# Performance work log

Hardware: AMD Instinct MI355X
Metric: run time of the kernel (lower is better)

Reference implementation:

```python
import math
import jax
import jax.numpy as jnp
import numpy as np

KS = 7  # kernel_size


def _make_cdt_kernel():
    # kornia.create_meshgrid(k,k,normalized=False) -> coords; centered; hypot -> exp(d/-0.35)
    r = np.arange(KS, dtype=np.float32) - (KS // 2)
    yy, xx = np.meshgrid(r, r, indexing="ij")
    k = np.exp(np.hypot(xx, yy) / -0.35)
    return jnp.asarray(k, jnp.float32)[None, None]  # (1,1,KS,KS) OIHW


def setup_inputs() -> dict:
    key = jax.random.key(0)
    B, C, H, W = 32, 3, 256, 256
    u = jax.random.uniform(key, (B, C, H, W), dtype=jnp.float32)
    image = (u < 0.005).astype(jnp.float32)
    return {"image": image}


def reference(image):
    B, C, H, W = image.shape
    kernel = _make_cdt_kernel()
    n_iters = math.ceil(max(H, W) / (KS // 2))  # static
    x = image.reshape(B * C, 1, H, W)
    out0 = jnp.zeros_like(x)

    def step(carry, i):
        out, boundary = carry
        conv = jax.lax.conv_general_dilated(
            boundary, kernel, (1, 1), "SAME",
            dimension_numbers=("NCHW", "OIHW", "NCHW"))
        # -0.35*log(conv) with posinf (conv==0) replaced by 0, exactly as
        # torch.nan_to_num(cdt, posinf=0.0); safe-log form avoids inf/nan.
        pos = conv > 0
        cdt = jnp.where(pos, -0.35 * jnp.log(jnp.where(pos, conv, 1.0)), 0.0)
        mask = cdt > 0
        offset = i.astype(jnp.float32) * (KS / 2)  # i * kernel_size / 2 (true div)
        out = out + jnp.where(mask, offset + cdt, 0.0)
        boundary = jnp.where(mask, 1.0, boundary)
        return (out, boundary), None

    (out, _), _ = jax.lax.scan(step, (out0, x), jnp.arange(n_iters))
    return out.reshape(B, C, H, W)
```

## Files before the change

kernel.cpp:

```cpp
#include <hip/hip_runtime.h>


typedef unsigned short u16x4 __attribute__((ext_vector_type(4)));

#define BIGV (1 << 20)
#define ROWB 272
#define CHB (256 * ROWB)

__global__ __launch_bounds__(256) void k_rowdist(const float* __restrict__ img,
                                                 unsigned char* __restrict__ d1) {
  const int lane = threadIdx.x & 63;
  const int wv = threadIdx.x >> 6;
  const int row = blockIdx.x * 4 + wv;
  const int x0 = lane * 4;

  const float4 v = *reinterpret_cast<const float4*>(&img[(size_t)row * 256 + x0]);

  int c0 = (v.x != 0.0f) ? -x0 : BIGV;
  int c1 = (v.y != 0.0f) ? -(x0 + 1) : BIGV;
  int c2 = (v.z != 0.0f) ? -(x0 + 2) : BIGV;
  int c3 = (v.w != 0.0f) ? -(x0 + 3) : BIGV;
  const int p0 = c0;
  const int p1 = min(c1, p0);
  const int p2 = min(c2, p1);
  const int p3 = min(c3, p2);
  int incl = p3;
#pragma unroll
  for (int off = 1; off < 64; off <<= 1) {
    int o = __shfl_up(incl, off, 64);
    if (lane >= off) incl = min(incl, o);
  }
  int excl = __shfl_up(incl, 1, 64);
  if (lane == 0) excl = BIGV;
  const int df0 = x0 + min(p0, excl);
  const int df1 = x0 + 1 + min(p1, excl);
  const int df2 = x0 + 2 + min(p2, excl);
  const int df3 = x0 + 3 + min(p3, excl);

  int g0 = (v.x != 0.0f) ? x0 : BIGV;
  int g1 = (v.y != 0.0f) ? (x0 + 1) : BIGV;
  int g2 = (v.z != 0.0f) ? (x0 + 2) : BIGV;
  int g3 = (v.w != 0.0f) ? (x0 + 3) : BIGV;
  const int q3 = g3;
  const int q2 = min(g2, q3);
  const int q1 = min(g1, q2);
  const int q0 = min(g0, q1);
  int incl2 = q0;
#pragma unroll
  for (int off = 1; off < 64; off <<= 1) {
    int o = __shfl_down(incl2, off, 64);
    if (lane < 64 - off) incl2 = min(incl2, o);
  }
  int excl2 = __shfl_down(incl2, 1, 64);
  if (lane == 63) excl2 = BIGV;
  const int db0 = min(q0, excl2) - x0;
  const int db1 = min(q1, excl2) - (x0 + 1);
  const int db2 = min(q2, excl2) - (x0 + 2);
  const int db3 = min(q3, excl2) - (x0 + 3);

  const unsigned int d0 = (unsigned int)min(min(df0, db0), 127);
  const unsigned int d1v = (unsigned int)min(min(df1, db1), 127);
  const unsigned int d2 = (unsigned int)min(min(df2, db2), 127);
  const unsigned int d3 = (unsigned int)min(min(df3, db3), 127);
  const int ch = row >> 8, y = row & 255;
  const size_t base = (size_t)ch * CHB + (size_t)y * ROWB;
  *reinterpret_cast<unsigned int*>(&d1[base + 8 + x0]) =
      d0 | (d1v << 8) | (d2 << 16) | (d3 << 24);
  if (lane < 2)
    *reinterpret_cast<unsigned int*>(&d1[base + lane * 4]) = 0u;
  else if (lane >= 62)
    *reinterpret_cast<unsigned int*>(&d1[base + 264 + (lane - 62) * 4]) = 0u;
}

#define TAPROW(s_, t_, A0, A1, A2, A3, A4, A5, A6)                              \
  do {                                                                          \
    const unsigned int r0_ = R[(s_) + (t_)][0];                                 \
    const unsigned int r1_ = R[(s_) + (t_)][1];                                 \
    const unsigned int r2_ = R[(s_) + (t_)][2];                                 \
    A0 += (((__builtin_amdgcn_alignbyte(r1_, r0_, 1) + Cp) & 0x80808080u) >> 7);\
    A1 += (((__builtin_amdgcn_alignbyte(r1_, r0_, 2) + Cp) & 0x80808080u) >> 7);\
    A2 += (((__builtin_amdgcn_alignbyte(r1_, r0_, 3) + Cp) & 0x80808080u) >> 7);\
    A3 += (((r1_ + Cp) & 0x80808080u) >> 7);                                    \
    A4 += (((__builtin_amdgcn_alignbyte(r2_, r1_, 1) + Cp) & 0x80808080u) >> 7);\
    A5 += (((__builtin_amdgcn_alignbyte(r2_, r1_, 2) + Cp) & 0x80808080u) >> 7);\
    A6 += (((__builtin_amdgcn_alignbyte(r2_, r1_, 3) + Cp) & 0x80808080u) >> 7);\
  } while (0)

#define TAPROWC(s_, t_, A0, A1, A2, A4, A5, A6)   \
  do {                                                                          \
    const unsigned int r0_ = R[(s_) + (t_)][0];                                 \
    const unsigned int r1_ = R[(s_) + (t_)][1];                                 \
    const unsigned int r2_ = R[(s_) + (t_)][2];                                 \
    A0 += (((__builtin_amdgcn_alignbyte(r1_, r0_, 1) + Cp) & 0x80808080u) >> 7);\
    A1 += (((__builtin_amdgcn_alignbyte(r1_, r0_, 2) + Cp) & 0x80808080u) >> 7);\
    A2 += (((__builtin_amdgcn_alignbyte(r1_, r0_, 3) + Cp) & 0x80808080u) >> 7);\
    A4 += (((__builtin_amdgcn_alignbyte(r2_, r1_, 1) + Cp) & 0x80808080u) >> 7);\
    A5 += (((__builtin_amdgcn_alignbyte(r2_, r1_, 2) + Cp) & 0x80808080u) >> 7);\
    A6 += (((__builtin_amdgcn_alignbyte(r2_, r1_, 3) + Cp) & 0x80808080u) >> 7);\
  } while (0)

#define EPI(s_)                                                                 \
  do {                                                                          \
    const unsigned int Dc = R[(s_) + 3][1];                                     \
    const int d0_ = (int)(Dc & 255u);                                           \
    const int d1_ = (int)((Dc >> 8) & 255u);                                    \
    const int d2_ = (int)((Dc >> 16) & 255u);                                   \
    const int d3_ = (int)(Dc >> 24);                                            \
    const int i0_ = (max(d0_ - 1, 0) * 86) >> 8;      \
    const int i1_ = (max(d1_ - 1, 0) * 86) >> 8;                                \
    const int i2_ = (max(d2_ - 1, 0) * 86) >> 8;                                \
    const int i3_ = (max(d3_ - 1, 0) * 86) >> 8;                                \
    const unsigned int Cp = (unsigned int)(127 - 3 * i0_) |                     \
                            ((unsigned int)(127 - 3 * i1_) << 8) |              \
                            ((unsigned int)(127 - 3 * i2_) << 16) |             \
                            ((unsigned int)(127 - 3 * i3_) << 24);              \
    unsigned int aA = 0, aB = 0, aC = 0, aD = 0;                                \
    TAPROW(s_, 0, aD, aD, aC, aC, aC, aD, aD);                                  \
    TAPROW(s_, 1, aD, aC, aB, aB, aB, aC, aD);                                  \
    TAPROW(s_, 2, aC, aB, aA, aA, aA, aB, aC);                                  \
    TAPROWC(s_, 3, aC, aB, aA, aA, aB, aC);                                     \
    TAPROW(s_, 4, aC, aB, aA, aA, aA, aB, aC);                                  \
    TAPROW(s_, 5, aD, aC, aB, aB, aB, aC, aD);                                  \
    TAPROW(s_, 6, aD, aD, aC, aC, aC, aD, aD);                                  \
    const float s0_ = fmaf((float)(aA & 255u), wA,                              \
                     fmaf((float)(aB & 255u), wB,                               \
                     fmaf((float)(aC & 255u), wC, (float)(aD & 255u) * wD)));   \
    const float s1_ = fmaf((float)((aA >> 8) & 255u), wA,                       \
                     fmaf((float)((aB >> 8) & 255u), wB,                        \
                     fmaf((float)((aC >> 8) & 255u), wC,                        \
                          (float)((aD >> 8) & 255u) * wD)));                    \
    const float s2_ = fmaf((float)((aA >> 16) & 255u), wA,                      \
                     fmaf((float)((aB >> 16) & 255u), wB,                       \
                     fmaf((float)((aC >> 16) & 255u), wC,                       \
                          (float)((aD >> 16) & 255u) * wD)));                   \
    const float s3_ = fmaf((float)(aA >> 24), wA,                               \
                     fmaf((float)(aB >> 24), wB,                                \
                     fmaf((float)(aC >> 24), wC, (float)(aD >> 24) * wD)));     \
    const float cv0_ = W4 - s0_, cv1_ = W4 - s1_;                               \
    const float cv2_ = W4 - s2_, cv3_ = W4 - s3_;                               \
    const float e0_ = fmaf(3.5f, (float)i0_, -0.35f * __logf(fmaxf(cv0_, 1e-30f))); \
    const float e1_ = fmaf(3.5f, (float)i1_, -0.35f * __logf(fmaxf(cv1_, 1e-30f))); \
    const float e2_ = fmaf(3.5f, (float)i2_, -0.35f * __logf(fmaxf(cv2_, 1e-30f))); \
    const float e3_ = fmaf(3.5f, (float)i3_, -0.35f * __logf(fmaxf(cv3_, 1e-30f))); \
    const float4 o4_ = make_float4(                                             \
        (d0_ > 0 && cv0_ > 1e-6f) ? e0_ : 0.0f,                                 \
        (d1_ > 0 && cv1_ > 1e-6f) ? e1_ : 0.0f,                                 \
        (d2_ > 0 && cv2_ > 1e-6f) ? e2_ : 0.0f,                                 \
        (d3_ > 0 && cv3_ > 1e-6f) ? e3_ : 0.0f);                                \
    *reinterpret_cast<float4*>(&out[obase + (size_t)(s_) * 256]) = o4_;         \
  } while (0)

#define LDQ(off) (*reinterpret_cast<const u16x4*>(&s1[(off)]))
#define EMIN __builtin_elementwise_min
#define EMAX __builtin_elementwise_max

__global__ __launch_bounds__(256) void k_fused(const unsigned char* __restrict__ d1,
                                               float* __restrict__ out) {
  const int ch = blockIdx.z;
  const int yt = blockIdx.y;
  const int xt = blockIdx.x;
  const int x0 = xt * 32;
  const int y0 = yt * 128;
  const int tid = threadIdx.x;
  const int lastxt = (int)gridDim.x - 1;

  __shared__ __align__(16) unsigned char s1[256 * 96];
  __shared__ __align__(16) unsigned char Ds[134 * 44];

  const unsigned char* src = d1 + (size_t)ch * CHB + x0;
#pragma unroll
  for (int it = 0; it < 3; ++it) {
    const int idx = it * 256 + tid;
    const int y = (idx * 21846) >> 16;
    const int seg = idx - y * 3;
    const uint4 q = *reinterpret_cast<const uint4*>(&src[y * ROWB + seg * 16]);
    uint4 lo, hi;
    lo.x = __builtin_amdgcn_perm(0u, q.x, 0x0C010C00u);
    lo.y = __builtin_amdgcn_perm(0u, q.x, 0x0C030C02u);
    lo.z = __builtin_amdgcn_perm(0u, q.y, 0x0C010C00u);
    lo.w = __builtin_amdgcn_perm(0u, q.y, 0x0C030C02u);
    hi.x = __builtin_amdgcn_perm(0u, q.z, 0x0C010C00u);
    hi.y = __builtin_amdgcn_perm(0u, q.z, 0x0C030C02u);
    hi.z = __builtin_amdgcn_perm(0u, q.w, 0x0C010C00u);
    hi.w = __builtin_amdgcn_perm(0u, q.w, 0x0C030C02u);
    *reinterpret_cast<uint4*>(&s1[y * 96 + seg * 32]) = lo;
    *reinterpret_cast<uint4*>(&s1[y * 96 + seg * 32 + 16]) = hi;
  }
  __syncthreads();

  const u16x4 K1 = {1, 1, 1, 1}, K2 = {2, 2, 2, 2}, K3 = {3, 3, 3, 3},
              K4 = {4, 4, 4, 4}, K5 = {5, 5, 5, 5}, K6 = {6, 6, 6, 6},
              K7 = {7, 7, 7, 7}, K8 = {8, 8, 8, 8};
#pragma unroll 1
  for (int it = 0; it < 6; ++it) {
    const int idx = it * 256 + tid;
    if (idx >= 1340) break;
    const int r = (idx * 6554) >> 16;
    const int g = idx - r * 10;
    const int y = y0 + r - 3;
    const bool ghost =
        (xt == 0 && g == 0) || (xt == lastxt && g == 9) || y < 0 || y > 255;
    if (ghost) {
      *reinterpret_cast<unsigned int*>(&Ds[r * 44 + g * 4]) = 0x7F7F7F7Fu;
      continue;
    }
    const int jb = 8 + 8 * g;
    const int rb = y * 96 + jb;
    const int bot = 255 * 96 + jb;
    const u16x4 b0 = LDQ(rb);
    const u16x4 u1 = LDQ(max(rb - 96, jb));
    const u16x4 u2 = LDQ(max(rb - 192, jb));
    const u16x4 u3 = LDQ(max(rb - 288, jb));
    const u16x4 u4 = LDQ(max(rb - 384, jb));
    const u16x4 u5 = LDQ(max(rb - 480, jb));
    const u16x4 u6 = LDQ(max(rb - 576, jb));
    const u16x4 u7 = LDQ(max(rb - 672, jb));
    const u16x4 u8 = LDQ(max(rb - 768, jb));
    const u16x4 w1 = LDQ(min(rb + 96, bot));
    const u16x4 w2 = LDQ(min(rb + 192, bot));
    const u16x4 w3 = LDQ(min(rb + 288, bot));
    const u16x4 w4 = LDQ(min(rb + 384, bot));
    const u16x4 w5 = LDQ(min(rb + 480, bot));
    const u16x4 w6 = LDQ(min(rb + 576, bot));
    const u16x4 w7 = LDQ(min(rb + 672, bot));
    const u16x4 w8 = LDQ(min(rb + 768, bot));
    const u16x4 mu = EMIN(EMIN(EMIN(EMAX(u1, K1), EMAX(u2, K2)),
                                EMIN(EMAX(u3, K3), EMAX(u4, K4))),
                          EMIN(EMIN(EMAX(u5, K5), EMAX(u6, K6)),
                                EMIN(EMAX(u7, K7), EMAX(u8, K8))));
    const u16x4 mw = EMIN(EMIN(EMIN(EMAX(w1, K1), EMAX(w2, K2)),
                                EMIN(EMAX(w3, K3), EMAX(w4, K4))),
                          EMIN(EMIN(EMAX(w5, K5), EMAX(w6, K6)),
                                EMIN(EMAX(w7, K7), EMAX(w8, K8))));
    u16x4 b = EMIN(b0, EMIN(mu, mw));
    unsigned long long bb = __builtin_bit_cast(unsigned long long, b);
    unsigned int blo = (unsigned int)bb, bhi = (unsigned int)(bb >> 32);
    int bm = max(max((int)(blo & 0xFFFFu), (int)(blo >> 16)),
                 max((int)(bhi & 0xFFFFu), (int)(bhi >> 16)));
    int k = 9;
    int au = rb - 768, ad = rb + 768;
    while (k < bm) {
      const unsigned short t1 = (unsigned short)k, t2 = (unsigned short)(k + 1),
                           t3 = (unsigned short)(k + 2), t4 = (unsigned short)(k + 3);
      const u16x4 c1 = {t1, t1, t1, t1}, c2 = {t2, t2, t2, t2},
                  c3 = {t3, t3, t3, t3}, c4 = {t4, t4, t4, t4};
      const u16x4 a1 = LDQ(max(au - 96, jb));
      const u16x4 a2 = LDQ(max(au - 192, jb));
      const u16x4 a3 = LDQ(max(au - 288, jb));
      const u16x4 a4 = LDQ(max(au - 384, jb));
      const u16x4 e1 = LDQ(min(ad + 96, bot));
      const u16x4 e2 = LDQ(min(ad + 192, bot));
      const u16x4 e3 = LDQ(min(ad + 288, bot));
      const u16x4 e4 = LDQ(min(ad + 384, bot));
      const u16x4 t = EMIN(EMIN(EMIN(EMAX(a1, c1), EMAX(a2, c2)),
                                 EMIN(EMAX(a3, c3), EMAX(a4, c4))),
                           EMIN(EMIN(EMAX(e1, c1), EMAX(e2, c2)),
                                 EMIN(EMAX(e3, c3), EMAX(e4, c4))));
      b = EMIN(b, t);
      au -= 384;
      ad += 384;
      k += 4;
      bb = __builtin_bit_cast(unsigned long long, b);
      blo = (unsigned int)bb;
      bhi = (unsigned int)(bb >> 32);
      bm = max(max((int)(blo & 0xFFFFu), (int)(blo >> 16)),
               max((int)(bhi & 0xFFFFu), (int)(bhi >> 16)));
    }
    const unsigned int packed = __builtin_amdgcn_perm(bhi, blo, 0x06040200u);
    *reinterpret_cast<unsigned int*>(&Ds[r * 44 + g * 4]) = packed;
  }
  __syncthreads();

  const float wA = 3.17814e-2f, wB = 2.35426e-3f, wC = 1.91126e-4f, wD = 1.35150e-5f;
  const float W4 = 8.0f * wA + 12.0f * wB + 16.0f * wC + 12.0f * wD;

  const int cg = tid & 7;
  const int rg = tid >> 3;
  const int rl0 = rg * 4;
  const int jb2 = cg * 4;
  const size_t obase = (size_t)ch * 65536 + (size_t)(y0 + rl0) * 256 + x0 + cg * 4;

  unsigned int R[10][3];
#pragma unroll
  for (int u = 0; u < 10; ++u) {
    const unsigned char* p = &Ds[(rl0 + u) * 44 + jb2];
    R[u][0] = *reinterpret_cast<const unsigned int*>(p);
    R[u][1] = *reinterpret_cast<const unsigned int*>(p + 4);
    R[u][2] = *reinterpret_cast<const unsigned int*>(p + 8);
  }

  EPI(0); EPI(1); EPI(2); EPI(3);
}

extern "C" void kernel_launch(void* const* d_in, const int* in_sizes, int n_in,
                              void* d_out, int out_size, void* d_ws, size_t ws_size,
                              hipStream_t stream) {
  const float* img = (const float*)d_in[0];
  float* out = (float*)d_out;
  unsigned char* Dbuf = (unsigned char*)d_ws;

  const int total = in_sizes[0];
  const int nch = total >> 16;

  k_rowdist<<<dim3(nch * 64), dim3(256), 0, stream>>>(img, Dbuf);
  k_fused<<<dim3(8, 2, nch), dim3(256), 0, stream>>>(Dbuf, out);
}
```

Baseline: 45.93 us.

## Compute five column-distance rows per thread with shared sliding window loads

The vertical min-distance pass now has each thread handle five consecutive output rows. It loads a 21-row window of LDS data once and reuses it across the five rows, where before it did 17 separate loads per row. The LDS buffer gets padded ghost rows filled with a sentinel so the clamped max/min addressing is mostly gone. The trade is more registers and a larger LDS footprint, and the loop now runs 270 work items instead of 1340, which may leave many threads idle.

```diff
diff --git a/kernel.cpp b/kernel.cpp
--- a/kernel.cpp
+++ b/kernel.cpp
@@ -86,7 +86,7 @@
     A6 += (((__builtin_amdgcn_alignbyte(r2_, r1_, 3) + Cp) & 0x80808080u) >> 7);\
   } while (0)
 
-#define TAPROWC(s_, t_, A0, A1, A2, A4, A5, A6)   \
+#define TAPROWC(s_, t_, A0, A1, A2, A4, A5, A6)                                 \
   do {                                                                          \
     const unsigned int r0_ = R[(s_) + (t_)][0];                                 \
     const unsigned int r1_ = R[(s_) + (t_)][1];                                 \
@@ -106,7 +106,7 @@
     const int d1_ = (int)((Dc >> 8) & 255u);                                    \
     const int d2_ = (int)((Dc >> 16) & 255u);                                   \
     const int d3_ = (int)(Dc >> 24);                                            \
-    const int i0_ = (max(d0_ - 1, 0) * 86) >> 8;      \
+    const int i0_ = (max(d0_ - 1, 0) * 86) >> 8;                                \
     const int i1_ = (max(d1_ - 1, 0) * 86) >> 8;                                \
     const int i2_ = (max(d2_ - 1, 0) * 86) >> 8;                                \
     const int i3_ = (max(d3_ - 1, 0) * 86) >> 8;                                \
@@ -125,10 +125,10 @@
     const float s0_ = fmaf((float)(aA & 255u), wA,                              \
                      fmaf((float)(aB & 255u), wB,                               \
                      fmaf((float)(aC & 255u), wC, (float)(aD & 255u) * wD)));   \
-    const float s1_ = fmaf((float)((aA >> 8) & 255u), wA,                       \
-                     fmaf((float)((aB >> 8) & 255u), wB,                        \
-                     fmaf((float)((aC >> 8) & 255u), wC,                        \
-                          (float)((aD >> 8) & 255u) * wD)));                    \
+    const float s1f_ = fmaf((float)((aA >> 8) & 255u), wA,                      \
+                      fmaf((float)((aB >> 8) & 255u), wB,                       \
+                      fmaf((float)((aC >> 8) & 255u), wC,                       \
+                           (float)((aD >> 8) & 255u) * wD)));                   \
     const float s2_ = fmaf((float)((aA >> 16) & 255u), wA,                      \
                      fmaf((float)((aB >> 16) & 255u), wB,                       \
                      fmaf((float)((aC >> 16) & 255u), wC,                       \
@@ -136,7 +136,7 @@
     const float s3_ = fmaf((float)(aA >> 24), wA,                               \
                      fmaf((float)(aB >> 24), wB,                                \
                      fmaf((float)(aC >> 24), wC, (float)(aD >> 24) * wD)));     \
-    const float cv0_ = W4 - s0_, cv1_ = W4 - s1_;                               \
+    const float cv0_ = W4 - s0_, cv1_ = W4 - s1f_;                              \
     const float cv2_ = W4 - s2_, cv3_ = W4 - s3_;                               \
     const float e0_ = fmaf(3.5f, (float)i0_, -0.35f * __logf(fmaxf(cv0_, 1e-30f))); \
     const float e1_ = fmaf(3.5f, (float)i1_, -0.35f * __logf(fmaxf(cv1_, 1e-30f))); \
@@ -154,6 +154,33 @@
 #define EMIN __builtin_elementwise_min
 #define EMAX __builtin_elementwise_max
 
+#define PFX(OUT, a0, a1, a2, a3, a4, a5, a6, a7, a8, a9, a10, a11, a12, a13,    \
+            a14, a15, a16)                                                      \
+  u16x4 OUT = EMIN(                                                             \
+      EMIN(EMIN(EMIN(EMAX(a7, K1), EMAX(a9, K1)),                               \
+                EMIN(EMAX(a6, K2), EMAX(a10, K2))),                             \
+           EMIN(EMIN(EMAX(a5, K3), EMAX(a11, K3)),                              \
+                EMIN(EMAX(a4, K4), EMAX(a12, K4)))),                            \
+      EMIN(EMIN(EMIN(EMAX(a3, K5), EMAX(a13, K5)),                              \
+                EMIN(EMAX(a2, K6), EMAX(a14, K6))),                             \
+           EMIN(EMIN(EMAX(a1, K7), EMAX(a15, K7)),                              \
+                EMIN(EMAX(a0, K8), EMAX(a16, K8)))));                           \
+  OUT = EMIN(OUT, a8)
+
+#define TUP(OUT, b3, b2, b1, b0, d0, d1, d2, d3)                                \
+  OUT = EMIN(OUT, EMIN(EMIN(EMIN(EMAX(b3, Kc0), EMAX(b2, Kc1)),                 \
+                            EMIN(EMAX(b1, Kc2), EMAX(b0, Kc3))),                \
+                       EMIN(EMIN(EMAX(d0, Kc0), EMAX(d1, Kc1)),                 \
+                            EMIN(EMAX(d2, Kc2), EMAX(d3, Kc3)))))
+
+#define BMOF(MX)                                                                \
+  ({                                                                            \
+    const unsigned long long mb_ = __builtin_bit_cast(unsigned long long, MX);  \
+    const unsigned int ml_ = (unsigned int)mb_, mh_ = (unsigned int)(mb_ >> 32);\
+    max(max((int)(ml_ & 0xFFFFu), (int)(ml_ >> 16)),                            \
+        max((int)(mh_ & 0xFFFFu), (int)(mh_ >> 16)));                           \
+  })
+
 __global__ __launch_bounds__(256) void k_fused(const unsigned char* __restrict__ d1,
                                                float* __restrict__ out) {
   const int ch = blockIdx.z;
@@ -164,9 +191,15 @@
   const int tid = threadIdx.x;
   const int lastxt = (int)gridDim.x - 1;
 
-  __shared__ __align__(16) unsigned char s1[256 * 96];
-  __shared__ __align__(16) unsigned char Ds[134 * 44];
-
+  __shared__ __align__(16) unsigned char s1[279 * 96];
+  __shared__ __align__(16) unsigned char Ds[136 * 44];
+
+  for (int i = tid; i < 552; i += 256) {
+    const int r = (i * 2731) >> 16;
+    const int c = i - r * 24;
+    const int row = (r < 11) ? r : r + 256;
+    *reinterpret_cast<unsigned int*>(&s1[row * 96 + c * 4]) = 0x007F007Fu;
+  }
   const unsigned char* src = d1 + (size_t)ch * CHB + x0;
 #pragma unroll
   for (int it = 0; it < 3; ++it) {
@@ -183,8 +216,8 @@
     hi.y = __builtin_amdgcn_perm(0u, q.z, 0x0C030C02u);
     hi.z = __builtin_amdgcn_perm(0u, q.w, 0x0C010C00u);
     hi.w = __builtin_amdgcn_perm(0u, q.w, 0x0C030C02u);
-    *reinterpret_cast<uint4*>(&s1[y * 96 + seg * 32]) = lo;
-    *reinterpret_cast<uint4*>(&s1[y * 96 + seg * 32 + 16]) = hi;
+    *reinterpret_cast<uint4*>(&s1[(y + 11) * 96 + seg * 32]) = lo;
+    *reinterpret_cast<uint4*>(&s1[(y + 11) * 96 + seg * 32 + 16]) = hi;
   }
   __syncthreads();
 
@@ -192,82 +225,72 @@
               K4 = {4, 4, 4, 4}, K5 = {5, 5, 5, 5}, K6 = {6, 6, 6, 6},
               K7 = {7, 7, 7, 7}, K8 = {8, 8, 8, 8};
 #pragma unroll 1
-  for (int it = 0; it < 6; ++it) {
-    const int idx = it * 256 + tid;
-    if (idx >= 1340) break;
-    const int r = (idx * 6554) >> 16;
-    const int g = idx - r * 10;
-    const int y = y0 + r - 3;
-    const bool ghost =
-        (xt == 0 && g == 0) || (xt == lastxt && g == 9) || y < 0 || y > 255;
-    if (ghost) {
-      *reinterpret_cast<unsigned int*>(&Ds[r * 44 + g * 4]) = 0x7F7F7F7Fu;
+  for (int t = tid; t < 270; t += 256) {
+    const int rg5 = (t * 6554) >> 16;
+    const int g = t - rg5 * 10;
+    const int r0r = rg5 * 5;
+    const int ybase = y0 + r0r - 3;
+    const int dsb = r0r * 44 + g * 4;
+    if ((xt == 0 && g == 0) || (xt == lastxt && g == 9)) {
+      *reinterpret_cast<unsigned int*>(&Ds[dsb]) = 0x7F7F7F7Fu;
+      *reinterpret_cast<unsigned int*>(&Ds[dsb + 44]) = 0x7F7F7F7Fu;
+      *reinterpret_cast<unsigned int*>(&Ds[dsb + 88]) = 0x7F7F7F7Fu;
+      *reinterpret_cast<unsigned int*>(&Ds[dsb + 132]) = 0x7F7F7F7Fu;
+      *reinterpret_cast<unsigned int*>(&Ds[dsb + 176]) = 0x7F7F7F7Fu;
       continue;
     }
     const int jb = 8 + 8 * g;
-    const int rb = y * 96 + jb;
-    const int bot = 255 * 96 + jb;
-    const u16x4 b0 = LDQ(rb);
-    const u16x4 u1 = LDQ(max(rb - 96, jb));
-    const u16x4 u2 = LDQ(max(rb - 192, jb));
-    const u16x4 u3 = LDQ(max(rb - 288, jb));
-    const u16x4 u4 = LDQ(max(rb - 384, jb));
-    const u16x4 u5 = LDQ(max(rb - 480, jb));
-    const u16x4 u6 = LDQ(max(rb - 576, jb));
-    const u16x4 u7 = LDQ(max(rb - 672, jb));
-    const u16x4 u8 = LDQ(max(rb - 768, jb));
-    const u16x4 w1 = LDQ(min(rb + 96, bot));
-    const u16x4 w2 = LDQ(min(rb + 192, bot));
-    const u16x4 w3 = LDQ(min(rb + 288, bot));
-    const u16x4 w4 = LDQ(min(rb + 384, bot));
-    const u16x4 w5 = LDQ(min(rb + 480, bot));
-    const u16x4 w6 = LDQ(min(rb + 576, bot));
-    const u16x4 w7 = LDQ(min(rb + 672, bot));
-    const u16x4 w8 = LDQ(min(rb + 768, bot));
-    const u16x4 mu = EMIN(EMIN(EMIN(EMAX(u1, K1), EMAX(u2, K2)),
-                                EMIN(EMAX(u3, K3), EMAX(u4, K4))),
-                          EMIN(EMIN(EMAX(u5, K5), EMAX(u6, K6)),
-                                EMIN(EMAX(u7, K7), EMAX(u8, K8))));
-    const u16x4 mw = EMIN(EMIN(EMIN(EMAX(w1, K1), EMAX(w2, K2)),
-                                EMIN(EMAX(w3, K3), EMAX(w4, K4))),
-                          EMIN(EMIN(EMAX(w5, K5), EMAX(w6, K6)),
-                                EMIN(EMAX(w7, K7), EMAX(w8, K8))));
-    u16x4 b = EMIN(b0, EMIN(mu, mw));
-    unsigned long long bb = __builtin_bit_cast(unsigned long long, b);
-    unsigned int blo = (unsigned int)bb, bhi = (unsigned int)(bb >> 32);
-    int bm = max(max((int)(blo & 0xFFFFu), (int)(blo >> 16)),
-                 max((int)(bhi & 0xFFFFu), (int)(bhi >> 16)));
-    int k = 9;
-    int au = rb - 768, ad = rb + 768;
-    while (k < bm) {
-      const unsigned short t1 = (unsigned short)k, t2 = (unsigned short)(k + 1),
-                           t3 = (unsigned short)(k + 2), t4 = (unsigned short)(k + 3);
-      const u16x4 c1 = {t1, t1, t1, t1}, c2 = {t2, t2, t2, t2},
-                  c3 = {t3, t3, t3, t3}, c4 = {t4, t4, t4, t4};
-      const u16x4 a1 = LDQ(max(au - 96, jb));
-      const u16x4 a2 = LDQ(max(au - 192, jb));
-      const u16x4 a3 = LDQ(max(au - 288, jb));
-      const u16x4 a4 = LDQ(max(au - 384, jb));
-      const u16x4 e1 = LDQ(min(ad + 96, bot));
-      const u16x4 e2 = LDQ(min(ad + 192, bot));
-      const u16x4 e3 = LDQ(min(ad + 288, bot));
-      const u16x4 e4 = LDQ(min(ad + 384, bot));
-      const u16x4 t = EMIN(EMIN(EMIN(EMAX(a1, c1), EMAX(a2, c2)),
-                                 EMIN(EMAX(a3, c3), EMAX(a4, c4))),
-                           EMIN(EMIN(EMAX(e1, c1), EMAX(e2, c2)),
-                                 EMIN(EMAX(e3, c3), EMAX(e4, c4))));
-      b = EMIN(b, t);
-      au -= 384;
-      ad += 384;
-      k += 4;
-      bb = __builtin_bit_cast(unsigned long long, b);
-      blo = (unsigned int)bb;
-      bhi = (unsigned int)(bb >> 32);
-      bm = max(max((int)(blo & 0xFFFFu), (int)(blo >> 16)),
-               max((int)(bhi & 0xFFFFu), (int)(bhi >> 16)));
+    const int ab = (ybase + 3) * 96 + jb;
+    const u16x4 w0 = LDQ(ab), w1 = LDQ(ab + 96), w2 = LDQ(ab + 192),
+                w3 = LDQ(ab + 288), w4 = LDQ(ab + 384), w5 = LDQ(ab + 480),
+                w6 = LDQ(ab + 576), w7 = LDQ(ab + 672), w8 = LDQ(ab + 768),
+                w9 = LDQ(ab + 864), w10 = LDQ(ab + 960), w11 = LDQ(ab + 1056),
+                w12 = LDQ(ab + 1152), w13 = LDQ(ab + 1248), w14 = LDQ(ab + 1344),
+                w15 = LDQ(ab + 1440), w16 = LDQ(ab + 1536), w17 = LDQ(ab + 1632),
+                w18 = LDQ(ab + 1728), w19 = LDQ(ab + 1824), w20 = LDQ(ab + 1920);
+    PFX(o0, w0, w1, w2, w3, w4, w5, w6, w7, w8, w9, w10, w11, w12, w13, w14, w15, w16);
+    PFX(o1, w1, w2, w3, w4, w5, w6, w7, w8, w9, w10, w11, w12, w13, w14, w15, w16, w17);
+    PFX(o2, w2, w3, w4, w5, w6, w7, w8, w9, w10, w11, w12, w13, w14, w15, w16, w17, w18);
+    PFX(o3, w3, w4, w5, w6, w7, w8, w9, w10, w11, w12, w13, w14, w15, w16, w17, w18, w19);
+    PFX(o4, w4, w5, w6, w7, w8, w9, w10, w11, w12, w13, w14, w15, w16, w17, w18, w19, w20);
+    u16x4 mx = EMAX(EMAX(o0, o1), EMAX(EMAX(o2, o3), o4));
+    int bm = BMOF(mx);
+    int kc = 9;
+    while (kc < bm) {
+      const unsigned short q0 = (unsigned short)kc, q1 = (unsigned short)(kc + 1),
+                           q2 = (unsigned short)(kc + 2), q3 = (unsigned short)(kc + 3);
+      const u16x4 Kc0 = {q0, q0, q0, q0}, Kc1 = {q1, q1, q1, q1},
+                  Kc2 = {q2, q2, q2, q2}, Kc3 = {q3, q3, q3, q3};
+      const int lo = jb, hi = 278 * 96 + jb;
+      const int aup = (ybase - kc + 8) * 96 + jb;
+      const int adn = (ybase + kc + 11) * 96 + jb;
+      const u16x4 t0 = LDQ(max(aup, lo)), t1 = LDQ(max(aup + 96, lo)),
+                  t2 = LDQ(max(aup + 192, lo)), t3 = LDQ(max(aup + 288, lo)),
+                  t4 = LDQ(max(aup + 384, lo)), t5 = LDQ(max(aup + 480, lo)),
+                  t6 = LDQ(max(aup + 576, lo)), t7 = LDQ(max(aup + 672, lo));
+      const u16x4 u0 = LDQ(min(adn, hi)), u1 = LDQ(min(adn + 96, hi)),
+                  u2 = LDQ(min(adn + 192, hi)), u3 = LDQ(min(adn + 288, hi)),
+                  u4 = LDQ(min(adn + 384, hi)), u5 = LDQ(min(adn + 480, hi)),
+                  u6 = LDQ(min(adn + 576, hi)), u7 = LDQ(min(adn + 672, hi));
+      TUP(o0, t3, t2, t1, t0, u0, u1, u2, u3);
+      TUP(o1, t4, t3, t2, t1, u1, u2, u3, u4);
+      TUP(o2, t5, t4, t3, t2, u2, u3, u4, u5);
+      TUP(o3, t6, t5, t4, t3, u3, u4, u5, u6);
+      TUP(o4, t7, t6, t5, t4, u4, u5, u6, u7);
+      kc += 4;
+      mx = EMAX(EMAX(o0, o1), EMAX(EMAX(o2, o3), o4));
+      bm = BMOF(mx);
     }
-    const unsigned int packed = __builtin_amdgcn_perm(bhi, blo, 0x06040200u);
-    *reinterpret_cast<unsigned int*>(&Ds[r * 44 + g * 4]) = packed;
+#define STROW(j_, OJ)                                                           \
+    {                                                                           \
+      const unsigned long long ob = __builtin_bit_cast(unsigned long long, OJ); \
+      unsigned int packed = __builtin_amdgcn_perm(                              \
+          (unsigned int)(ob >> 32), (unsigned int)ob, 0x06040200u);             \
+      if ((unsigned int)(ybase + (j_)) > 255u) packed = 0x7F7F7F7Fu;            \
+      *reinterpret_cast<unsigned int*>(&Ds[dsb + (j_) * 44]) = packed;          \
+    }
+    STROW(0, o0); STROW(1, o1); STROW(2, o2); STROW(3, o3); STROW(4, o4);
+#undef STROW
   }
   __syncthreads();
 
```

Measured after the change: 46.44 us. Within noise of the previous version (+1.1%).
